# Kernel optimization log

Hardware: AMD Instinct MI355X
Metric: run time of the kernel (lower is better)

The kernel has to match this reference:

```python
import jax, jax.numpy as jnp
import numpy as np

NB = 4          # bits per symbol (QAM16)
K = 3           # num_streams
M = 8           # rx antennas
B = 4096        # batch
NPTS = 2 ** NB  # constellation points per stream
C = NPTS ** K   # exhaustive candidate vectors


def _pam_gray(b):
    if len(b) > 1:
        return (1 - 2 * b[0]) * (2 ** len(b[1:]) - _pam_gray(b[1:]))
    return 1 - 2 * b[0]


def _qam_points(nb):
    # Gray-labeled QAM, normalized to unit average energy (as sionna's Constellation)
    n = 2 ** nb
    pts = np.zeros(n, np.complex64)
    for i in range(n):
        b = np.array(list(np.binary_repr(i, nb)), int)
        pts[i] = _pam_gray(b[0::2]) + 1j * _pam_gray(b[1::2])
    pts /= np.sqrt(np.mean(np.abs(pts) ** 2)).astype(np.float32)
    return pts.astype(np.complex64)


def _candidates():
    pts = _qam_points(NB)
    idx = np.arange(C)
    # per-stream symbol indices, stream 0 is most significant (vec_list order)
    sym_idx = np.stack([(idx // NPTS ** (K - 1 - k)) % NPTS for k in range(K)], axis=1)  # [C,K]
    xc = pts[sym_idx]  # [C,K] complex candidate symbol vectors
    # bits: MSB-first per symbol -> [C, K, NB]
    bits = ((sym_idx[..., None] >> (NB - 1 - np.arange(NB))) & 1).astype(bool)
    return xc, bits.reshape(C, K * NB)


_XC, _BITS = _candidates()


def setup_inputs() -> dict:
    key = jax.random.key(0)
    ks = jax.random.split(key, 6)
    y_re = jax.random.normal(ks[0], (B, M), jnp.float32)
    y_im = jax.random.normal(ks[1], (B, M), jnp.float32)
    h_re = jax.random.normal(ks[2], (B, M, K), jnp.float32)
    h_im = jax.random.normal(ks[3], (B, M, K), jnp.float32)
    # Hermitian PD noise covariance S = F F^H / M + 2 I
    fr = jax.random.normal(ks[4], (B, M, M), jnp.float32)
    fi = jax.random.normal(ks[5], (B, M, M), jnp.float32)
    F = fr + 1j * fi
    S = jnp.einsum('bij,bkj->bik', F, F.conj()) / M + 2.0 * jnp.eye(M, dtype=jnp.complex64)
    return {"y_re": y_re, "y_im": y_im, "h_re": h_re, "h_im": h_im,
            "s_re": jnp.real(S), "s_im": jnp.imag(S)}


def reference(y_re, y_im, h_re, h_im, s_re, s_im):
    y = y_re + 1j * y_im            # [B,M]
    h = h_re + 1j * h_im            # [B,M,K]
    s = s_re + 1j * s_im            # [B,M,M] Hermitian PD
    # Whiten: L L^H = S ; ||L^{-1}(y - Hx)||^2 = (y-Hx)^H S^{-1} (y-Hx)
    L = jnp.linalg.cholesky(s)
    yw = jax.scipy.linalg.solve_triangular(L, y[..., None], lower=True)[..., 0]  # [B,M]
    hw = jax.scipy.linalg.solve_triangular(L, h, lower=True)                     # [B,M,K]

    xc = jnp.asarray(_XC)                         # [C,K]
    G = jnp.einsum('bmk,bml->bkl', hw.conj(), hw)  # [B,K,K] Gram
    z = jnp.einsum('bm,bmk->bk', yw.conj(), hw)    # [B,K]  y~^H H~
    P = xc.conj()[:, :, None] * xc[:, None, :]     # [C,K,K] candidate outer products
    quad = jnp.real(jnp.einsum('bkl,ckl->bc', G, P))   # x^H G x
    cross = jnp.real(jnp.einsum('bk,ck->bc', z, xc))   # Re(y~^H H~ x)
    yn = jnp.sum(jnp.abs(yw) ** 2, axis=-1, keepdims=True)
    d = yn - 2.0 * cross + quad                   # [B,C] exhaustive squared distances

    # maxlog bit LLRs: LLR = min_{bit=0} d - min_{bit=1} d
    bits = jnp.asarray(_BITS)                     # [C, K*NB] bool
    BIG = jnp.float32(1e30)
    llrs = []
    for p in range(K * NB):  # fixed small loop over bit positions
        mask = bits[:, p]
        min1 = jnp.min(jnp.where(mask, d, BIG), axis=1)
        min0 = jnp.min(jnp.where(mask, BIG, d), axis=1)
        llrs.append(min0 - min1)
    return jnp.stack(llrs, axis=-1).reshape(B, K, NB)
```

## Files before the change

kernel.cpp:

```cpp
#include <hip/hip_runtime.h>
#include <math.h>

#define BIG 1e30f

__device__ __forceinline__ constexpr float QR(int i) {
    return ((((i >> 3) & 1) ? -1.0f : 1.0f) * ((((i >> 1) & 1) ? 3.0f : 1.0f)) *
            0.31622776601683794f);
}
__device__ __forceinline__ constexpr float QI(int i) {
    return ((((i >> 2) & 1) ? -1.0f : 1.0f) * (((i & 1) ? 3.0f : 1.0f)) *
            0.31622776601683794f);
}

__global__ __launch_bounds__(64, 1) void prep_kernel(
    const float* __restrict__ y_re, const float* __restrict__ y_im,
    const float* __restrict__ h_re, const float* __restrict__ h_im,
    const float* __restrict__ s_re, const float* __restrict__ s_im,
    float* __restrict__ ws, int B) {
    int b = blockIdx.x * blockDim.x + threadIdx.x;
    if (b >= B) return;
    const float* Sr = s_re + b * 64;
    const float* Si = s_im + b * 64;

    float Lr[8][8], Li[8][8], dinv[8];
#pragma unroll
    for (int i = 0; i < 8; ++i) {
#pragma unroll
        for (int j = 0; j < 8; ++j) {
            if (j < i) {
                float ar = Sr[i * 8 + j], ai = Si[i * 8 + j];
#pragma unroll
                for (int k = 0; k < 8; ++k) {
                    if (k < j) {
                        ar -= Lr[i][k] * Lr[j][k] + Li[i][k] * Li[j][k];
                        ai -= Li[i][k] * Lr[j][k] - Lr[i][k] * Li[j][k];
                    }
                }
                Lr[i][j] = ar * dinv[j];
                Li[i][j] = ai * dinv[j];
            }
        }
        float dd = Sr[i * 8 + i];
#pragma unroll
        for (int k = 0; k < 8; ++k) {
            if (k < i) dd -= Lr[i][k] * Lr[i][k] + Li[i][k] * Li[i][k];
        }
        float sq = sqrtf(dd);
        dinv[i] = 1.0f / sq;
    }

    float ywr[8], ywi[8];
#pragma unroll
    for (int i = 0; i < 8; ++i) {
        float ar = y_re[b * 8 + i], ai = y_im[b * 8 + i];
#pragma unroll
        for (int k = 0; k < 8; ++k) {
            if (k < i) {
                ar -= Lr[i][k] * ywr[k] - Li[i][k] * ywi[k];
                ai -= Lr[i][k] * ywi[k] + Li[i][k] * ywr[k];
            }
        }
        ywr[i] = ar * dinv[i];
        ywi[i] = ai * dinv[i];
    }

    float hwr[8][3], hwi[8][3];
#pragma unroll
    for (int c = 0; c < 3; ++c) {
#pragma unroll
        for (int i = 0; i < 8; ++i) {
            float ar = h_re[b * 24 + i * 3 + c], ai = h_im[b * 24 + i * 3 + c];
#pragma unroll
            for (int k = 0; k < 8; ++k) {
                if (k < i) {
                    ar -= Lr[i][k] * hwr[k][c] - Li[i][k] * hwi[k][c];
                    ai -= Lr[i][k] * hwi[k][c] + Li[i][k] * hwr[k][c];
                }
            }
            hwr[i][c] = ar * dinv[i];
            hwi[i][c] = ai * dinv[i];
        }
    }

    float g00 = 0, g11 = 0, g22 = 0;
    float g01r = 0, g01i = 0, g02r = 0, g02i = 0, g12r = 0, g12i = 0;
    float z0r = 0, z0i = 0, z1r = 0, z1i = 0, z2r = 0, z2i = 0;
#pragma unroll
    for (int m = 0; m < 8; ++m) {
        float a0r = hwr[m][0], a0i = hwi[m][0];
        float a1r = hwr[m][1], a1i = hwi[m][1];
        float a2r = hwr[m][2], a2i = hwi[m][2];
        g00 += a0r * a0r + a0i * a0i;
        g11 += a1r * a1r + a1i * a1i;
        g22 += a2r * a2r + a2i * a2i;
        g01r += a0r * a1r + a0i * a1i;
        g01i += a0r * a1i - a0i * a1r;
        g02r += a0r * a2r + a0i * a2i;
        g02i += a0r * a2i - a0i * a2r;
        g12r += a1r * a2r + a1i * a2i;
        g12i += a1r * a2i - a1i * a2r;
        float yr = ywr[m], yi = ywi[m];
        z0r += yr * a0r + yi * a0i;
        z0i += yr * a0i - yi * a0r;
        z1r += yr * a1r + yi * a1i;
        z1i += yr * a1i - yi * a1r;
        z2r += yr * a2r + yi * a2i;
        z2i += yr * a2i - yi * a2r;
    }
    float* o = ws + b * 16;
    o[0] = g00;  o[1] = g11;  o[2] = g22;
    o[3] = g01r; o[4] = g01i; o[5] = g02r; o[6] = g02i; o[7] = g12r; o[8] = g12i;
    o[9] = z0r;  o[10] = z0i; o[11] = z1r; o[12] = z1i; o[13] = z2r; o[14] = z2i;
    o[15] = 0.0f;
}

__global__ __launch_bounds__(256, 1) void mld_search(const float* __restrict__ ws,
                                                     float* __restrict__ out) {
    int b = blockIdx.x;
    int tid = threadIdx.x;
    const float* w = ws + b * 16;
    float g00 = w[0], g11 = w[1], g22 = w[2];
    float g01r = w[3], g01i = w[4], g02r = w[5], g02i = w[6], g12r = w[7], g12i = w[8];
    float z0r = w[9], z0i = w[10], z1r = w[11], z1i = w[12], z2r = w[13], z2i = w[14];

    int i0 = tid >> 4, i1 = tid & 15;
    float p0r = QR(i0), p0i = QI(i0);
    float p1r = QR(i1), p1i = QI(i1);
    float n0 = p0r * p0r + p0i * p0i;
    float n1 = p1r * p1r + p1i * p1i;

    float a0 = g00 * n0 - 2.0f * (z0r * p0r - z0i * p0i);
    float a1 = g11 * n1 - 2.0f * (z1r * p1r - z1i * p1i);
    float crr = p0r * p1r + p0i * p1i;
    float cri = p0r * p1i - p0i * p1r;
    float base = a0 + a1 + 2.0f * (g01r * crr - g01i * cri);
    float w0r = g02r * p0r + g02i * p0i;
    float w0i = g02i * p0r - g02r * p0i;
    float w1r = g12r * p1r + g12i * p1i;
    float w1i = g12i * p1r - g12r * p1i;
    float cr = 2.0f * (w0r + w1r - z2r);
    float ci = -2.0f * (w0i + w1i - z2i);

    float m2[8];
#pragma unroll
    for (int j = 0; j < 8; ++j) m2[j] = BIG;
#pragma unroll
    for (int i2 = 0; i2 < 16; ++i2) {
        float pr = QR(i2), pi = QI(i2);
        float d = base + g22 * (pr * pr + pi * pi) + cr * pr + ci * pi;
        m2[0 + ((i2 >> 3) & 1)] = fminf(m2[0 + ((i2 >> 3) & 1)], d);
        m2[2 + ((i2 >> 2) & 1)] = fminf(m2[2 + ((i2 >> 2) & 1)], d);
        m2[4 + ((i2 >> 1) & 1)] = fminf(m2[4 + ((i2 >> 1) & 1)], d);
        m2[6 + (i2 & 1)]        = fminf(m2[6 + (i2 & 1)], d);
    }
    float tmin = fminf(m2[0], m2[1]);

    __shared__ float s_tmin[256];
    __shared__ float s_r[32];
    __shared__ float s_m2[32];
    s_tmin[tid] = tmin;

#pragma unroll
    for (int j = 0; j < 8; ++j) {
        float v = m2[j];
#pragma unroll
        for (int mask = 1; mask < 64; mask <<= 1) v = fminf(v, __shfl_xor(v, mask, 64));
        m2[j] = v;
    }
    int wave = tid >> 6, lane = tid & 63;
    if (lane == 0) {
#pragma unroll
        for (int j = 0; j < 8; ++j) s_m2[wave * 8 + j] = m2[j];
    }
    __syncthreads();

    if (tid < 16) {
        float m = BIG;
#pragma unroll
        for (int j = 0; j < 16; ++j) m = fminf(m, s_tmin[tid * 16 + j]);
        s_r[tid] = m;
    } else if (tid < 32) {
        int i1x = tid - 16;
        float m = BIG;
#pragma unroll
        for (int j = 0; j < 16; ++j) m = fminf(m, s_tmin[j * 16 + i1x]);
        s_r[16 + i1x] = m;
    }
    __syncthreads();

    if (tid < 12) {
        int k = tid >> 2, n = tid & 3, sh = 3 - n;
        float m0 = BIG, m1 = BIG;
        if (k < 2) {
            const float* r = s_r + k * 16;
#pragma unroll
            for (int j = 0; j < 16; ++j) {
                float v = r[j];
                if ((j >> sh) & 1) m1 = fminf(m1, v);
                else m0 = fminf(m0, v);
            }
        } else {
#pragma unroll
            for (int wv = 0; wv < 4; ++wv) {
                m0 = fminf(m0, s_m2[wv * 8 + n * 2 + 0]);
                m1 = fminf(m1, s_m2[wv * 8 + n * 2 + 1]);
            }
        }
        out[b * 12 + tid] = m0 - m1;
    }
}

extern "C" void kernel_launch(void* const* d_in, const int* in_sizes, int n_in,
                              void* d_out, int out_size, void* d_ws, size_t ws_size,
                              hipStream_t stream) {
    const float* y_re = (const float*)d_in[0];
    const float* y_im = (const float*)d_in[1];
    const float* h_re = (const float*)d_in[2];
    const float* h_im = (const float*)d_in[3];
    const float* s_re = (const float*)d_in[4];
    const float* s_im = (const float*)d_in[5];
    int B = in_sizes[0] / 8;
    float* ws = (float*)d_ws;

    prep_kernel<<<dim3((B + 63) / 64), dim3(64), 0, stream>>>(y_re, y_im, h_re, h_im,
                                                              s_re, s_im, ws, B);
    mld_search<<<dim3(B), dim3(256), 0, stream>>>(ws, (float*)d_out);
}
```

Before: 81.50 us.

## Fuse Cholesky prep into search kernel with wave-parallel shuffle-based factorization

After: 82.10 us. Within noise of the previous version (+0.7%).

```diff
diff --git a/kernel.cpp b/kernel.cpp
--- a/kernel.cpp
+++ b/kernel.cpp
@@ -12,116 +12,88 @@
             0.31622776601683794f);
 }
 
-__global__ __launch_bounds__(64, 1) void prep_kernel(
+__global__ __launch_bounds__(256, 1) void mld_fused(
     const float* __restrict__ y_re, const float* __restrict__ y_im,
     const float* __restrict__ h_re, const float* __restrict__ h_im,
     const float* __restrict__ s_re, const float* __restrict__ s_im,
-    float* __restrict__ ws, int B) {
-    int b = blockIdx.x * blockDim.x + threadIdx.x;
-    if (b >= B) return;
-    const float* Sr = s_re + b * 64;
-    const float* Si = s_im + b * 64;
+    float* __restrict__ out) {
+    int b = blockIdx.x;
+    int tid = threadIdx.x;
 
-    float Lr[8][8], Li[8][8], dinv[8];
-#pragma unroll
-    for (int i = 0; i < 8; ++i) {
+    __shared__ float s_xr[4][8], s_xi[4][8];
+    __shared__ float s_w[16];
+    __shared__ float s_tmin[256];
+    __shared__ float s_r[32];
+    __shared__ float s_m2[32];
+
+    if (tid < 64) {
+        int ii = tid >> 3, kk = tid & 7;
+        float ar = s_re[b * 64 + tid];
+        float ai = s_im[b * 64 + tid];
+        float br = 0.0f, bi = 0.0f;
+        if (kk == 0) {
+            br = y_re[b * 8 + ii];
+            bi = y_im[b * 8 + ii];
+        } else if (kk < 4) {
+            br = h_re[b * 24 + ii * 3 + (kk - 1)];
+            bi = h_im[b * 24 + ii * 3 + (kk - 1)];
+        }
+
 #pragma unroll
         for (int j = 0; j < 8; ++j) {
-            if (j < i) {
-                float ar = Sr[i * 8 + j], ai = Si[i * 8 + j];
-#pragma unroll
-                for (int k = 0; k < 8; ++k) {
-                    if (k < j) {
-                        ar -= Lr[i][k] * Lr[j][k] + Li[i][k] * Li[j][k];
-                        ai -= Li[i][k] * Lr[j][k] - Lr[i][k] * Li[j][k];
-                    }
-                }
-                Lr[i][j] = ar * dinv[j];
-                Li[i][j] = ai * dinv[j];
+            float djr = __shfl(ar, j * 9, 64);
+            float dinv = 1.0f / sqrtf(djr);
+            if (kk == j && ii >= j) { ar *= dinv; ai *= dinv; }
+            float Lijr = __shfl(ar, ii * 8 + j, 64), Liji = __shfl(ai, ii * 8 + j, 64);
+            float Lkjr = __shfl(ar, kk * 8 + j, 64), Lkji = __shfl(ai, kk * 8 + j, 64);
+            if (kk > j && ii >= kk) {
+                ar -= Lijr * Lkjr + Liji * Lkji;
+                ai -= Liji * Lkjr - Lijr * Lkji;
             }
         }
-        float dd = Sr[i * 8 + i];
+
 #pragma unroll
         for (int k = 0; k < 8; ++k) {
-            if (k < i) dd -= Lr[i][k] * Lr[i][k] + Li[i][k] * Li[i][k];
-        }
-        float sq = sqrtf(dd);
-        dinv[i] = 1.0f / sq;
-    }
-
-    float ywr[8], ywi[8];
-#pragma unroll
-    for (int i = 0; i < 8; ++i) {
-        float ar = y_re[b * 8 + i], ai = y_im[b * 8 + i];
-#pragma unroll
-        for (int k = 0; k < 8; ++k) {
-            if (k < i) {
-                ar -= Lr[i][k] * ywr[k] - Li[i][k] * ywi[k];
-                ai -= Lr[i][k] * ywi[k] + Li[i][k] * ywr[k];
+            float dk = __shfl(ar, k * 9, 64);
+            float dinvk = 1.0f / dk;
+            if (ii == k) { br *= dinvk; bi *= dinvk; }
+            float xkr = __shfl(br, k * 8 + kk, 64), xki = __shfl(bi, k * 8 + kk, 64);
+            float Likr = __shfl(ar, ii * 8 + k, 64), Liki = __shfl(ai, ii * 8 + k, 64);
+            if (ii > k) {
+                br -= Likr * xkr - Liki * xki;
+                bi -= Likr * xki + Liki * xkr;
             }
         }
-        ywr[i] = ar * dinv[i];
-        ywi[i] = ai * dinv[i];
+        if (kk < 4) { s_xr[kk][ii] = br; s_xi[kk][ii] = bi; }
     }
+    __syncthreads();
 
-    float hwr[8][3], hwi[8][3];
+    if (tid < 9) {
+        int a = (int)((0x000211321ull >> (tid * 4)) & 15ull);
+        int c = (int)((0x321332321ull >> (tid * 4)) & 15ull);
+        float sr = 0.0f, si = 0.0f;
 #pragma unroll
-    for (int c = 0; c < 3; ++c) {
-#pragma unroll
-        for (int i = 0; i < 8; ++i) {
-            float ar = h_re[b * 24 + i * 3 + c], ai = h_im[b * 24 + i * 3 + c];
-#pragma unroll
-            for (int k = 0; k < 8; ++k) {
-                if (k < i) {
-                    ar -= Lr[i][k] * hwr[k][c] - Li[i][k] * hwi[k][c];
-                    ai -= Lr[i][k] * hwi[k][c] + Li[i][k] * hwr[k][c];
-                }
-            }
-            hwr[i][c] = ar * dinv[i];
-            hwi[i][c] = ai * dinv[i];
+        for (int m = 0; m < 8; ++m) {
+            float xar = s_xr[a][m], xai = s_xi[a][m];
+            float xbr = s_xr[c][m], xbi = s_xi[c][m];
+            sr += xar * xbr + xai * xbi;
+            si += xar * xbi - xai * xbr;
+        }
+        if (tid < 3) {
+            s_w[tid] = sr;
+        } else {
+            int base = 3 + (tid - 3) * 2;
+            s_w[base] = sr;
+            s_w[base + 1] = si;
         }
     }
+    __syncthreads();
 
-    float g00 = 0, g11 = 0, g22 = 0;
-    float g01r = 0, g01i = 0, g02r = 0, g02i = 0, g12r = 0, g12i = 0;
-    float z0r = 0, z0i = 0, z1r = 0, z1i = 0, z2r = 0, z2i = 0;
-#pragma unroll
-    for (int m = 0; m < 8; ++m) {
-        float a0r = hwr[m][0], a0i = hwi[m][0];
-        float a1r = hwr[m][1], a1i = hwi[m][1];
-        float a2r = hwr[m][2], a2i = hwi[m][2];
-        g00 += a0r * a0r + a0i * a0i;
-        g11 += a1r * a1r + a1i * a1i;
-        g22 += a2r * a2r + a2i * a2i;
-        g01r += a0r * a1r + a0i * a1i;
-        g01i += a0r * a1i - a0i * a1r;
-        g02r += a0r * a2r + a0i * a2i;
-        g02i += a0r * a2i - a0i * a2r;
-        g12r += a1r * a2r + a1i * a2i;
-        g12i += a1r * a2i - a1i * a2r;
-        float yr = ywr[m], yi = ywi[m];
-        z0r += yr * a0r + yi * a0i;
-        z0i += yr * a0i - yi * a0r;
-        z1r += yr * a1r + yi * a1i;
-        z1i += yr * a1i - yi * a1r;
-        z2r += yr * a2r + yi * a2i;
-        z2i += yr * a2i - yi * a2r;
-    }
-    float* o = ws + b * 16;
-    o[0] = g00;  o[1] = g11;  o[2] = g22;
-    o[3] = g01r; o[4] = g01i; o[5] = g02r; o[6] = g02i; o[7] = g12r; o[8] = g12i;
-    o[9] = z0r;  o[10] = z0i; o[11] = z1r; o[12] = z1i; o[13] = z2r; o[14] = z2i;
-    o[15] = 0.0f;
-}
-
-__global__ __launch_bounds__(256, 1) void mld_search(const float* __restrict__ ws,
-                                                     float* __restrict__ out) {
-    int b = blockIdx.x;
-    int tid = threadIdx.x;
-    const float* w = ws + b * 16;
-    float g00 = w[0], g11 = w[1], g22 = w[2];
-    float g01r = w[3], g01i = w[4], g02r = w[5], g02i = w[6], g12r = w[7], g12i = w[8];
-    float z0r = w[9], z0i = w[10], z1r = w[11], z1i = w[12], z2r = w[13], z2i = w[14];
+    float g00 = s_w[0], g11 = s_w[1], g22 = s_w[2];
+    float g01r = s_w[3], g01i = s_w[4], g02r = s_w[5], g02i = s_w[6];
+    float g12r = s_w[7], g12i = s_w[8];
+    float z0r = s_w[9], z0i = s_w[10], z1r = s_w[11], z1i = s_w[12];
+    float z2r = s_w[13], z2i = s_w[14];
 
     int i0 = tid >> 4, i1 = tid & 15;
     float p0r = QR(i0), p0i = QI(i0);
@@ -155,9 +127,6 @@
     }
     float tmin = fminf(m2[0], m2[1]);
 
-    __shared__ float s_tmin[256];
-    __shared__ float s_r[32];
-    __shared__ float s_m2[32];
     s_tmin[tid] = tmin;
 
 #pragma unroll
@@ -220,9 +189,7 @@
     const float* s_re = (const float*)d_in[4];
     const float* s_im = (const float*)d_in[5];
     int B = in_sizes[0] / 8;
-    float* ws = (float*)d_ws;
 
-    prep_kernel<<<dim3((B + 63) / 64), dim3(64), 0, stream>>>(y_re, y_im, h_re, h_im,
-                                                              s_re, s_im, ws, B);
-    mld_search<<<dim3(B), dim3(256), 0, stream>>>(ws, (float*)d_out);
+    mld_fused<<<dim3(B), dim3(256), 0, stream>>>(y_re, y_im, h_re, h_im, s_re, s_im,
+                                                 (float*)d_out);
 }
```
